# Kernel optimization log

Hardware: AMD Instinct MI355X
Metric: run time of the kernel (lower is better)

Reference implementation:

```python
import jax, jax.numpy as jnp
import numpy as np

EPS = 1e-8  # torch cosine_similarity clamps norms at 1e-8
TEMPERATURE = 0.05


def _normalize(x):
    n = jnp.linalg.norm(x, axis=-1, keepdims=True)
    return x / jnp.maximum(n, EPS)


def setup_inputs() -> dict:
    key = jax.random.key(0)
    k1, k2, k3 = jax.random.split(key, 3)
    N, D = 8192, 256
    return {
        "text_embeddings": jax.random.normal(k1, (N, D), dtype=jnp.float32),
        "text_pos_embeddings": jax.random.normal(k2, (N, D), dtype=jnp.float32),
        "text_neg_embeddings": jax.random.normal(k3, (N, D), dtype=jnp.float32),
    }


def _pair_loss(a, b):
    # PairInBatchNegCoSentLoss(a, b): cos-sim matrix, scale, diag-subtract, LSE
    sim = _normalize(a) @ _normalize(b).T / TEMPERATURE  # [N, N]
    diff = sim - jnp.diagonal(sim)[:, None]
    return jax.nn.logsumexp(diff, axis=1).mean()


def reference(text_embeddings, text_pos_embeddings, text_neg_embeddings):
    e = _normalize(text_embeddings)
    p = _normalize(text_pos_embeddings)
    n = _normalize(text_neg_embeddings)
    sim_pos = jnp.sum(e * p, axis=-1)          # [N]
    sim_neg = e @ n.T                          # [N, N]
    sim = jnp.concatenate([sim_pos[:, None], sim_neg], axis=1) / TEMPERATURE
    diff = sim - sim[:, 0:1]
    loss = jax.nn.logsumexp(diff, axis=1).mean()
    # add_swap_loss=True: pair loss with (pos, anchor) swapped
    loss = loss + _pair_loss(text_pos_embeddings, text_embeddings)
    return loss
```

## Files before the change

kernel.cpp:

```cpp
#include <hip/hip_runtime.h>
#include <stdint.h>

#define N 8192
#define D 256
#define INV_T 20.0f
#define LOG2E 1.44269504088896340736f
#define BM 128
#define BN 128
#define NXB 64

typedef __attribute__((ext_vector_type(16))) float f32x16;
typedef __attribute__((ext_vector_type(4))) int i32x4;
typedef __attribute__((ext_vector_type(8))) int i32x8;

typedef __attribute__((address_space(3))) uint32_t lds_u32;
typedef __attribute__((address_space(1))) const uint32_t gbl_u32;

static __device__ __forceinline__ float fast_exp2(float x) {
#if __has_builtin(__builtin_amdgcn_exp2f)
  return __builtin_amdgcn_exp2f(x);
#else
  float r;
  asm("v_exp_f32 %0, %1" : "=v"(r) : "v"(x));
  return r;
#endif
}

#define DPP_ADD(v, ctrl)                                                      \
  ((v) + __builtin_bit_cast(float, __builtin_amdgcn_update_dpp(               \
             0, __builtin_bit_cast(int, (v)), (ctrl), 0xf, 0xf, true)))

__global__ __launch_bounds__(256) void normalize_kernel(
    const float* __restrict__ e, const float* __restrict__ p, const float* __restrict__ n,
    uint32_t* __restrict__ eb, uint32_t* __restrict__ pb, uint32_t* __restrict__ nb,
    float* __restrict__ cbuf) {
  const int tid = threadIdx.x;
  const int wave = tid >> 6, lane = tid & 63;
  const int row = blockIdx.x * 4 + wave;

  const float4 ev = ((const float4*)(e + (size_t)row * D))[lane];
  const float4 pv = ((const float4*)(p + (size_t)row * D))[lane];
  const float4 nv = ((const float4*)(n + (size_t)row * D))[lane];

  float sse = ev.x*ev.x + ev.y*ev.y + ev.z*ev.z + ev.w*ev.w;
  float ssp = pv.x*pv.x + pv.y*pv.y + pv.z*pv.z + pv.w*pv.w;
  float ssn = nv.x*nv.x + nv.y*nv.y + nv.z*nv.z + nv.w*nv.w;
  float dep = ev.x*pv.x + ev.y*pv.y + ev.z*pv.z + ev.w*pv.w;
#pragma unroll
  for (int m = 1; m < 64; m <<= 1) {
    sse += __shfl_xor(sse, m);
    ssp += __shfl_xor(ssp, m);
    ssn += __shfl_xor(ssn, m);
    dep += __shfl_xor(dep, m);
  }
  const float se = 1.0f / fmaxf(sqrtf(sse), 1e-8f);
  const float sp = 1.0f / fmaxf(sqrtf(ssp), 1e-8f);
  const float sn = 1.0f / fmaxf(sqrtf(ssn), 1e-8f);

  int ue = __builtin_amdgcn_cvt_pk_fp8_f32(ev.x*se, ev.y*se, 0, false);
  ue     = __builtin_amdgcn_cvt_pk_fp8_f32(ev.z*se, ev.w*se, ue, true);
  int up = __builtin_amdgcn_cvt_pk_fp8_f32(pv.x*sp, pv.y*sp, 0, false);
  up     = __builtin_amdgcn_cvt_pk_fp8_f32(pv.z*sp, pv.w*sp, up, true);
  int un = __builtin_amdgcn_cvt_pk_fp8_f32(nv.x*sn, nv.y*sn, 0, false);
  un     = __builtin_amdgcn_cvt_pk_fp8_f32(nv.z*sn, nv.w*sn, un, true);
  eb[row * 64 + lane] = (uint32_t)ue;
  pb[row * 64 + lane] = (uint32_t)up;
  nb[row * 64 + lane] = (uint32_t)un;

  if (lane == 0) cbuf[row] = dep * se * sp * INV_T;
}

__global__ __launch_bounds__(256, 3) void simexp_kernel(
    const uint8_t* __restrict__ eb, const uint8_t* __restrict__ pb,
    const uint8_t* __restrict__ nb, const float* __restrict__ cbuf,
    float* __restrict__ part) {
  __shared__ uint8_t Bs[BN * D];
  __shared__ float cs[BM];

  const int z = blockIdx.z;
  const uint8_t* __restrict__ A = z ? pb : eb;
  const uint8_t* __restrict__ B = z ? eb : nb;

  const int tid = threadIdx.x;
  const int wave = tid >> 6, lane = tid & 63;
  const int lane31 = lane & 31, half = lane >> 5;
  const int rowTile = blockIdx.x * BM, colblk = blockIdx.y;
  const int colTile = colblk * BN;

#pragma unroll
  for (int i = 0; i < 8; ++i) {
    const int c = i * 256 + tid, r = c >> 4, sl = c & 15;
    const int gg = sl ^ (r & 15);
    __builtin_amdgcn_global_load_lds(
        (gbl_u32*)(B + (size_t)(colTile + r) * D + gg * 16),
        (lds_u32*)&Bs[c * 16], 16, 0, 0);
  }

  const int arow = rowTile + wave * 32 + lane31;
  const uint8_t* __restrict__ Arow = A + (size_t)arow * D + half * 32;
  i32x8 afr[4];
#pragma unroll
  for (int s = 0; s < 4; ++s) {
    const i32x4 lo = *(const i32x4*)(Arow + s * 64);
    const i32x4 hi = *(const i32x4*)(Arow + s * 64 + 16);
    afr[s] = (i32x8){lo[0], lo[1], lo[2], lo[3], hi[0], hi[1], hi[2], hi[3]};
  }

  if (tid < BM) cs[tid] = cbuf[rowTile + tid] * LOG2E;

  int bbase[4];
#pragma unroll
  for (int ni = 0; ni < 4; ++ni) {
    const int cl = ni * 32 + lane31;
    bbase[ni] = (cl << 8) ^ ((cl & 15) << 4) ^ (half << 5);
  }

  f32x16 acc[4];
#pragma unroll
  for (int ni = 0; ni < 4; ++ni)
#pragma unroll
    for (int r = 0; r < 16; ++r) acc[ni][r] = 0.0f;

  __syncthreads();

#pragma unroll
  for (int s = 0; s < 4; ++s) {
#pragma unroll
    for (int ni = 0; ni < 4; ++ni) {
      const int alo = bbase[ni] ^ (s << 6);
      const i32x4 blo = *(const i32x4*)&Bs[alo];
      const i32x4 bhi = *(const i32x4*)&Bs[alo ^ 16];
      const i32x8 b = (i32x8){blo[0], blo[1], blo[2], blo[3],
                              bhi[0], bhi[1], bhi[2], bhi[3]};
      acc[ni] = __builtin_amdgcn_mfma_scale_f32_32x32x64_f8f6f4(
          afr[s], b, acc[ni],
          0 , 0 ,
          0, 0x7F7F7F7F , 0, 0x7F7F7F7F );
    }
  }

  const float K2 = INV_T * LOG2E;
#pragma unroll
  for (int reg = 0; reg < 16; ++reg) {
    const int rlocal = (reg & 3) + 8 * (reg >> 2) + 4 * half;
    const int rowl = wave * 32 + rlocal;
    const float cv = cs[rowl];
    float v = fast_exp2(acc[0][reg] * K2 - cv) + fast_exp2(acc[1][reg] * K2 - cv) +
              fast_exp2(acc[2][reg] * K2 - cv) + fast_exp2(acc[3][reg] * K2 - cv);
    v = DPP_ADD(v, 0xB1);
    v = DPP_ADD(v, 0x4E);
    v = DPP_ADD(v, 0x141);
    v = DPP_ADD(v, 0x140);
    v += __builtin_bit_cast(float, __builtin_amdgcn_ds_swizzle(
             __builtin_bit_cast(int, v), 0x401F));
    if (lane31 == 0)
      part[((size_t)(z * NXB + colblk)) * N + rowTile + rowl] = v;
  }
}

__global__ __launch_bounds__(64) void reduce1_kernel(const float* __restrict__ part,
                                                     float* __restrict__ partials) {
  const int bid = blockIdx.x;
  const int z = bid >> 7;
  const int row = (bid & 127) * 64 + threadIdx.x;
  float s = 0.0f;
#pragma unroll 8
  for (int x = 0; x < NXB; ++x)
    s += part[((size_t)(z * NXB + x)) * N + row];
  float val = z ? logf(s) : log1pf(s);
#pragma unroll
  for (int m = 1; m < 64; m <<= 1) val += __shfl_xor(val, m);
  if (threadIdx.x == 0) partials[bid] = val;
}

__global__ __launch_bounds__(256) void reduce2_kernel(const float* __restrict__ partials,
                                                      float* __restrict__ out) {
  const int tid = threadIdx.x;
  float v = partials[tid];
#pragma unroll
  for (int m = 1; m < 64; m <<= 1) v += __shfl_xor(v, m);
  __shared__ float sm[4];
  if ((tid & 63) == 0) sm[tid >> 6] = v;
  __syncthreads();
  if (tid == 0) out[0] = (sm[0] + sm[1] + sm[2] + sm[3]) * (1.0f / (float)N);
}

extern "C" void kernel_launch(void* const* d_in, const int* in_sizes, int n_in,
                              void* d_out, int out_size, void* d_ws, size_t ws_size,
                              hipStream_t stream) {
  const float* e = (const float*)d_in[0];
  const float* p = (const float*)d_in[1];
  const float* n = (const float*)d_in[2];

  char* w = (char*)d_ws;
  uint8_t* eb = (uint8_t*)w;
  uint8_t* pb = eb + (size_t)N * D;
  uint8_t* nb = pb + (size_t)N * D;
  float* cbuf = (float*)(nb + (size_t)N * D);
  float* part = cbuf + N;
  float* partials = part + (size_t)2 * NXB * N;

  normalize_kernel<<<N / 4, 256, 0, stream>>>(e, p, n, (uint32_t*)eb, (uint32_t*)pb,
                                              (uint32_t*)nb, cbuf);
  simexp_kernel<<<dim3(N / BM, N / BN, 2), 256, 0, stream>>>(eb, pb, nb, cbuf, part);
  reduce1_kernel<<<256, 64, 0, stream>>>(part, partials);
  reduce2_kernel<<<1, 256, 0, stream>>>(partials, (float*)d_out);
}
```

Baseline: 127.5 us.

## Make simexp blocks persistent over 16 column tiles with double-buffered LDS staging

Each block now covers one row tile and loops over 16 consecutive column tiles. The B tile for two iterations ahead is prefetched into a double-buffered LDS region while the current tile runs MFMA and exp. Row sums stay in registers across tiles, so the partial-sum buffer shrinks from 64 to 4 chunks per row and reduce1 does much less work. In exchange the grid drops from 8192 to 512 blocks, occupancy is capped at 2 blocks per CU, and two barriers per tile may serialize the pipeline.

```diff
diff --git a/kernel.cpp b/kernel.cpp
--- a/kernel.cpp
+++ b/kernel.cpp
@@ -7,7 +7,8 @@
 #define LOG2E 1.44269504088896340736f
 #define BM 128
 #define BN 128
-#define NXB 64
+#define NCHUNK 4
+#define NT 16
 
 typedef __attribute__((ext_vector_type(16))) float f32x16;
 typedef __attribute__((ext_vector_type(4))) int i32x4;
@@ -17,13 +18,9 @@
 typedef __attribute__((address_space(1))) const uint32_t gbl_u32;
 
 static __device__ __forceinline__ float fast_exp2(float x) {
-#if __has_builtin(__builtin_amdgcn_exp2f)
-  return __builtin_amdgcn_exp2f(x);
-#else
   float r;
   asm("v_exp_f32 %0, %1" : "=v"(r) : "v"(x));
   return r;
-#endif
 }
 
 #define DPP_ADD(v, ctrl)                                                      \
@@ -70,12 +67,11 @@
   if (lane == 0) cbuf[row] = dep * se * sp * INV_T;
 }
 
-__global__ __launch_bounds__(256, 3) void simexp_kernel(
+__global__ __launch_bounds__(256, 2) void simexp_kernel(
     const uint8_t* __restrict__ eb, const uint8_t* __restrict__ pb,
     const uint8_t* __restrict__ nb, const float* __restrict__ cbuf,
     float* __restrict__ part) {
-  __shared__ uint8_t Bs[BN * D];
-  __shared__ float cs[BM];
+  __shared__ uint8_t Bs[2][BN * D];
 
   const int z = blockIdx.z;
   const uint8_t* __restrict__ A = z ? pb : eb;
@@ -84,17 +80,21 @@
   const int tid = threadIdx.x;
   const int wave = tid >> 6, lane = tid & 63;
   const int lane31 = lane & 31, half = lane >> 5;
-  const int rowTile = blockIdx.x * BM, colblk = blockIdx.y;
-  const int colTile = colblk * BN;
-
-#pragma unroll
-  for (int i = 0; i < 8; ++i) {
-    const int c = i * 256 + tid, r = c >> 4, sl = c & 15;
-    const int gg = sl ^ (r & 15);
-    __builtin_amdgcn_global_load_lds(
-        (gbl_u32*)(B + (size_t)(colTile + r) * D + gg * 16),
-        (lds_u32*)&Bs[c * 16], 16, 0, 0);
-  }
+  const int chunk = blockIdx.x;
+  const int rowTile = blockIdx.y * BM;
+  const int colblk0 = chunk * NT;
+
+#define STAGEB(buf, cblk)                                                     \
+  do {                                                                        \
+    const uint8_t* __restrict__ Bsrc = B + (size_t)(cblk) * (BN * D);         \
+    _Pragma("unroll") for (int i = 0; i < 8; ++i) {                           \
+      const int c = i * 256 + tid, r = c >> 4, sl = c & 15;                   \
+      const int gg = sl ^ (r & 15);                                           \
+      __builtin_amdgcn_global_load_lds(                                       \
+          (gbl_u32*)(Bsrc + (size_t)r * D + gg * 16),                         \
+          (lds_u32*)&Bs[buf][c * 16], 16, 0, 0);                              \
+    }                                                                         \
+  } while (0)
 
   const int arow = rowTile + wave * 32 + lane31;
   const uint8_t* __restrict__ Arow = A + (size_t)arow * D + half * 32;
@@ -105,8 +105,14 @@
     const i32x4 hi = *(const i32x4*)(Arow + s * 64 + 16);
     afr[s] = (i32x8){lo[0], lo[1], lo[2], lo[3], hi[0], hi[1], hi[2], hi[3]};
   }
-
-  if (tid < BM) cs[tid] = cbuf[rowTile + tid] * LOG2E;
+  float cv[16];
+#pragma unroll
+  for (int reg = 0; reg < 16; ++reg)
+    cv[reg] = cbuf[rowTile + wave * 32 + (reg & 3) + 8 * (reg >> 2) + 4 * half] * LOG2E;
+
+  STAGEB(0, colblk0 + 0);
+  STAGEB(1, colblk0 + 1);
+  __builtin_amdgcn_sched_barrier(0);
 
   int bbase[4];
 #pragma unroll
@@ -115,46 +121,64 @@
     bbase[ni] = (cl << 8) ^ ((cl & 15) << 4) ^ (half << 5);
   }
 
-  f32x16 acc[4];
-#pragma unroll
-  for (int ni = 0; ni < 4; ++ni)
-#pragma unroll
-    for (int r = 0; r < 16; ++r) acc[ni][r] = 0.0f;
-
-  __syncthreads();
-
-#pragma unroll
-  for (int s = 0; s < 4; ++s) {
-#pragma unroll
-    for (int ni = 0; ni < 4; ++ni) {
-      const int alo = bbase[ni] ^ (s << 6);
-      const i32x4 blo = *(const i32x4*)&Bs[alo];
-      const i32x4 bhi = *(const i32x4*)&Bs[alo ^ 16];
-      const i32x8 b = (i32x8){blo[0], blo[1], blo[2], blo[3],
-                              bhi[0], bhi[1], bhi[2], bhi[3]};
-      acc[ni] = __builtin_amdgcn_mfma_scale_f32_32x32x64_f8f6f4(
-          afr[s], b, acc[ni],
-          0 , 0 ,
-          0, 0x7F7F7F7F , 0, 0x7F7F7F7F );
-    }
-  }
-
+  float sums[16];
+#pragma unroll
+  for (int reg = 0; reg < 16; ++reg) sums[reg] = 0.0f;
+
+  const uint8_t* __restrict__ bs = &Bs[0][0];
   const float K2 = INV_T * LOG2E;
+
+#define TILE_BODY(t, VCNT)                                                    \
+  do {                                                                        \
+    asm volatile("s_waitcnt vmcnt(" #VCNT ")" ::: "memory");                  \
+    __builtin_amdgcn_s_barrier();                                             \
+    __builtin_amdgcn_sched_barrier(0);                                        \
+    const int bpar = ((t) & 1) << 15;                                         \
+    f32x16 acc[4];                                                            \
+    _Pragma("unroll") for (int ni = 0; ni < 4; ++ni)                          \
+      _Pragma("unroll") for (int r = 0; r < 16; ++r) acc[ni][r] = 0.0f;       \
+    _Pragma("unroll") for (int s = 0; s < 4; ++s) {                           \
+      _Pragma("unroll") for (int ni = 0; ni < 4; ++ni) {                      \
+        const int alo = (bbase[ni] ^ bpar) ^ (s << 6);                        \
+        const i32x4 blo = *(const i32x4*)&bs[alo];                            \
+        const i32x4 bhi = *(const i32x4*)&bs[alo ^ 16];                       \
+        const i32x8 b = (i32x8){blo[0], blo[1], blo[2], blo[3],               \
+                                bhi[0], bhi[1], bhi[2], bhi[3]};              \
+        acc[ni] = __builtin_amdgcn_mfma_scale_f32_32x32x64_f8f6f4(            \
+            afr[s], b, acc[ni], 0, 0, 0, 0x7F7F7F7F, 0, 0x7F7F7F7F);          \
+      }                                                                       \
+    }                                                                         \
+    __builtin_amdgcn_sched_barrier(0);                                        \
+    __builtin_amdgcn_s_barrier();       \
+    __builtin_amdgcn_sched_barrier(0);                                        \
+    if ((t) + 2 < NT) STAGEB((t) & 1, colblk0 + (t) + 2);                     \
+    _Pragma("unroll") for (int reg = 0; reg < 16; ++reg) {                    \
+      sums[reg] += fast_exp2(acc[0][reg] * K2 - cv[reg]) +                    \
+                   fast_exp2(acc[1][reg] * K2 - cv[reg]) +                    \
+                   fast_exp2(acc[2][reg] * K2 - cv[reg]) +                    \
+                   fast_exp2(acc[3][reg] * K2 - cv[reg]);                     \
+    }                                                                         \
+  } while (0)
+
+#pragma unroll 1
+  for (int t = 0; t < NT - 1; ++t) TILE_BODY(t, 8);
+  TILE_BODY(NT - 1, 0);
+#undef TILE_BODY
+#undef STAGEB
+
 #pragma unroll
   for (int reg = 0; reg < 16; ++reg) {
-    const int rlocal = (reg & 3) + 8 * (reg >> 2) + 4 * half;
-    const int rowl = wave * 32 + rlocal;
-    const float cv = cs[rowl];
-    float v = fast_exp2(acc[0][reg] * K2 - cv) + fast_exp2(acc[1][reg] * K2 - cv) +
-              fast_exp2(acc[2][reg] * K2 - cv) + fast_exp2(acc[3][reg] * K2 - cv);
+    float v = sums[reg];
     v = DPP_ADD(v, 0xB1);
     v = DPP_ADD(v, 0x4E);
     v = DPP_ADD(v, 0x141);
     v = DPP_ADD(v, 0x140);
     v += __builtin_bit_cast(float, __builtin_amdgcn_ds_swizzle(
              __builtin_bit_cast(int, v), 0x401F));
-    if (lane31 == 0)
-      part[((size_t)(z * NXB + colblk)) * N + rowTile + rowl] = v;
+    if (lane31 == 0) {
+      const int rowl = wave * 32 + (reg & 3) + 8 * (reg >> 2) + 4 * half;
+      part[((size_t)(z * NCHUNK + chunk)) * N + rowTile + rowl] = v;
+    }
   }
 }
 
@@ -164,9 +188,9 @@
   const int z = bid >> 7;
   const int row = (bid & 127) * 64 + threadIdx.x;
   float s = 0.0f;
-#pragma unroll 8
-  for (int x = 0; x < NXB; ++x)
-    s += part[((size_t)(z * NXB + x)) * N + row];
+#pragma unroll
+  for (int x = 0; x < NCHUNK; ++x)
+    s += part[((size_t)(z * NCHUNK + x)) * N + row];
   float val = z ? logf(s) : log1pf(s);
 #pragma unroll
   for (int m = 1; m < 64; m <<= 1) val += __shfl_xor(val, m);
@@ -198,11 +222,11 @@
   uint8_t* nb = pb + (size_t)N * D;
   float* cbuf = (float*)(nb + (size_t)N * D);
   float* part = cbuf + N;
-  float* partials = part + (size_t)2 * NXB * N;
+  float* partials = part + (size_t)2 * NCHUNK * N;
 
   normalize_kernel<<<N / 4, 256, 0, stream>>>(e, p, n, (uint32_t*)eb, (uint32_t*)pb,
                                               (uint32_t*)nb, cbuf);
-  simexp_kernel<<<dim3(N / BM, N / BN, 2), 256, 0, stream>>>(eb, pb, nb, cbuf, part);
+  simexp_kernel<<<dim3(NCHUNK, N / BM, 2), 256, 0, stream>>>(eb, pb, nb, cbuf, part);
   reduce1_kernel<<<256, 64, 0, stream>>>(part, partials);
   reduce2_kernel<<<1, 256, 0, stream>>>(partials, (float*)d_out);
 }
```

After: 128.3 us. About the same (+0.6%).

## Accumulate row sums with atomics and merge reduction kernels into one finalize

Applied to the files above, without the earlier changes.

The simexp kernel now atomically adds each tile's per-row exp sums into a 2N row-sum buffer instead of writing a 2×64×N partial array. The buffer and output are zeroed inside the normalize kernel, and a single finalize kernel takes the logs and atomically adds into the output. This removes about 4 MB of partial-sum traffic and one kernel launch, at the cost of contended float atomics (64 per row) and non-deterministic summation order. The exp2 helper is also changed to always use inline asm.

```diff
diff --git a/kernel.cpp b/kernel.cpp
--- a/kernel.cpp
+++ b/kernel.cpp
@@ -17,13 +17,9 @@
 typedef __attribute__((address_space(1))) const uint32_t gbl_u32;
 
 static __device__ __forceinline__ float fast_exp2(float x) {
-#if __has_builtin(__builtin_amdgcn_exp2f)
-  return __builtin_amdgcn_exp2f(x);
-#else
   float r;
   asm("v_exp_f32 %0, %1" : "=v"(r) : "v"(x));
   return r;
-#endif
 }
 
 #define DPP_ADD(v, ctrl)                                                      \
@@ -33,10 +29,13 @@
 __global__ __launch_bounds__(256) void normalize_kernel(
     const float* __restrict__ e, const float* __restrict__ p, const float* __restrict__ n,
     uint32_t* __restrict__ eb, uint32_t* __restrict__ pb, uint32_t* __restrict__ nb,
-    float* __restrict__ cbuf) {
+    float* __restrict__ cbuf, float* __restrict__ srow, float* __restrict__ out) {
   const int tid = threadIdx.x;
   const int wave = tid >> 6, lane = tid & 63;
   const int row = blockIdx.x * 4 + wave;
+
+  if (tid < 8) srow[blockIdx.x * 8 + tid] = 0.0f;
+  if (blockIdx.x == 0 && tid == 0) out[0] = 0.0f;
 
   const float4 ev = ((const float4*)(e + (size_t)row * D))[lane];
   const float4 pv = ((const float4*)(p + (size_t)row * D))[lane];
@@ -73,7 +72,7 @@
 __global__ __launch_bounds__(256, 3) void simexp_kernel(
     const uint8_t* __restrict__ eb, const uint8_t* __restrict__ pb,
     const uint8_t* __restrict__ nb, const float* __restrict__ cbuf,
-    float* __restrict__ part) {
+    float* __restrict__ srow) {
   __shared__ uint8_t Bs[BN * D];
   __shared__ float cs[BM];
 
@@ -154,35 +153,18 @@
     v += __builtin_bit_cast(float, __builtin_amdgcn_ds_swizzle(
              __builtin_bit_cast(int, v), 0x401F));
     if (lane31 == 0)
-      part[((size_t)(z * NXB + colblk)) * N + rowTile + rowl] = v;
+      atomicAdd(&srow[(size_t)z * N + rowTile + rowl], v);
   }
 }
 
-__global__ __launch_bounds__(64) void reduce1_kernel(const float* __restrict__ part,
-                                                     float* __restrict__ partials) {
-  const int bid = blockIdx.x;
-  const int z = bid >> 7;
-  const int row = (bid & 127) * 64 + threadIdx.x;
-  float s = 0.0f;
-#pragma unroll 8
-  for (int x = 0; x < NXB; ++x)
-    s += part[((size_t)(z * NXB + x)) * N + row];
-  float val = z ? logf(s) : log1pf(s);
+__global__ __launch_bounds__(64) void finalize_kernel(const float* __restrict__ srow,
+                                                      float* __restrict__ out) {
+  const int r = blockIdx.x * 64 + threadIdx.x;
+  const float s = srow[r];
+  float val = (r >= N) ? logf(s) : log1pf(s);
 #pragma unroll
   for (int m = 1; m < 64; m <<= 1) val += __shfl_xor(val, m);
-  if (threadIdx.x == 0) partials[bid] = val;
-}
-
-__global__ __launch_bounds__(256) void reduce2_kernel(const float* __restrict__ partials,
-                                                      float* __restrict__ out) {
-  const int tid = threadIdx.x;
-  float v = partials[tid];
-#pragma unroll
-  for (int m = 1; m < 64; m <<= 1) v += __shfl_xor(v, m);
-  __shared__ float sm[4];
-  if ((tid & 63) == 0) sm[tid >> 6] = v;
-  __syncthreads();
-  if (tid == 0) out[0] = (sm[0] + sm[1] + sm[2] + sm[3]) * (1.0f / (float)N);
+  if (threadIdx.x == 0) atomicAdd(out, val * (1.0f / (float)N));
 }
 
 extern "C" void kernel_launch(void* const* d_in, const int* in_sizes, int n_in,
@@ -197,12 +179,11 @@
   uint8_t* pb = eb + (size_t)N * D;
   uint8_t* nb = pb + (size_t)N * D;
   float* cbuf = (float*)(nb + (size_t)N * D);
-  float* part = cbuf + N;
-  float* partials = part + (size_t)2 * NXB * N;
+  float* srow = cbuf + N;
 
   normalize_kernel<<<N / 4, 256, 0, stream>>>(e, p, n, (uint32_t*)eb, (uint32_t*)pb,
-                                              (uint32_t*)nb, cbuf);
-  simexp_kernel<<<dim3(N / BM, N / BN, 2), 256, 0, stream>>>(eb, pb, nb, cbuf, part);
-  reduce1_kernel<<<256, 64, 0, stream>>>(part, partials);
-  reduce2_kernel<<<1, 256, 0, stream>>>(partials, (float*)d_out);
+                                              (uint32_t*)nb, cbuf, srow,
+                                              (float*)d_out);
+  simexp_kernel<<<dim3(N / BM, N / BN, 2), 256, 0, stream>>>(eb, pb, nb, cbuf, srow);
+  finalize_kernel<<<256, 64, 0, stream>>>(srow, (float*)d_out);
 }
```

Result: no change. 126.9 us (-0.5%).
